# Kernel optimization log

Hardware: AMD Instinct MI355X
Metric: run time of the kernel (lower is better)

Reference implementation:

```python
import jax, jax.numpy as jnp
import numpy as np
import math

L = 16.0
DT = 1.0
TAU = 10.0
THRESHOLD = 1.0
ALPHA = 0.01
DECAY = math.exp(-DT / TAU)

@jax.custom_vjp
def multibit_spike(x):
    # forward: floor(x) clipped to [0, L]
    return jnp.clip(jnp.floor(x), 0.0, L)

def _spike_fwd(x):
    return multibit_spike(x), x

def _spike_bwd(x, g):
    dist = jnp.abs(x - jnp.round(x))
    scale = jnp.clip(1.0 - 2.0 * dist, 0.0, 1.0)
    in_range = ((x >= 0.0) & (x <= L + 1.0)).astype(g.dtype)
    return (g * in_range * scale,)

multibit_spike.defvjp(_spike_fwd, _spike_bwd)

def setup_inputs() -> dict:
    key = jax.random.key(0)
    k_x, k_w = jax.random.split(key)
    B, T, IN, H = 16, 2048, 512, 512
    # SNN-aware init: std = 0.5*threshold / (sqrt(fan_in)*0.3)
    std = 0.5 * THRESHOLD / (math.sqrt(IN) * 0.3)
    x = jax.random.normal(k_x, (B, T, IN), dtype=jnp.float32)
    W = jax.random.normal(k_w, (H, IN), dtype=jnp.float32) * std
    b = jnp.zeros((H,), dtype=jnp.float32)
    return {"x": x, "W": W, "b": b}

def reference(x, W, b):
    B, T, _ = x.shape
    Hd = W.shape[0]
    # batched linear projection of the whole sequence (compute-heavy GEMM)
    h = jnp.einsum('bti,hi->bth', x, W) + b  # [B, T, H]
    v0 = jnp.zeros((B, Hd), dtype=x.dtype)
    theta0 = jnp.full((B, Hd), THRESHOLD, dtype=x.dtype)

    def step(carry, i_t):
        v, theta = carry
        v = v * DECAY + i_t
        clamp_limit = L * theta * 2.0
        v = jnp.clip(v, -clamp_limit, clamp_limit)
        spike = multibit_spike(v / theta)
        v = v - spike * theta
        theta = theta + ALPHA * spike - ALPHA * (theta - THRESHOLD)
        return (v, theta), spike

    (v_f, theta_f), spikes_tbh = jax.lax.scan(step, (v0, theta0), jnp.swapaxes(h, 0, 1))
    spikes = jnp.swapaxes(spikes_tbh, 0, 1)  # [B, T, H]
    return spikes, v_f, theta_f
```

## Files before the change

kernel.cpp:

```cpp
#include <hip/hip_runtime.h>

#define B_  16
#define T_  2048
#define IN_ 512
#define H_  512
#define M_  (B_ * T_)

static __device__ __forceinline__ float4 ld4(const float* p) {
    return *reinterpret_cast<const float4*>(p);
}

#define BM 128
#define BN 128
#define BK 16
#define LDT (BM + 4)

__global__ __launch_bounds__(256)
void gemm_xwT(const float* __restrict__ X, const float* __restrict__ W,
              const float* __restrict__ bias, float* __restrict__ Hout) {
    __shared__ float As[BK][LDT];
    __shared__ float Bs[BK][LDT];

    const int tid = threadIdx.x;
    const int m0  = blockIdx.x * BM;
    const int n0  = blockIdx.y * BN;

    const int tx = tid & 15;
    const int ty = tid >> 4;

    const int row = tid >> 2;
    const int kph = (tid & 3) * 4;

    float acc[8][8];
#pragma unroll
    for (int i = 0; i < 8; ++i)
#pragma unroll
        for (int j = 0; j < 8; ++j) acc[i][j] = 0.0f;

    for (int k0 = 0; k0 < IN_; k0 += BK) {
        float4 a0 = ld4(&X[(size_t)(m0 + row)      * IN_ + k0 + kph]);
        float4 a1 = ld4(&X[(size_t)(m0 + row + 64) * IN_ + k0 + kph]);
        float4 b0 = ld4(&W[(size_t)(n0 + row)      * IN_ + k0 + kph]);
        float4 b1 = ld4(&W[(size_t)(n0 + row + 64) * IN_ + k0 + kph]);

        As[kph + 0][row]      = a0.x;  As[kph + 1][row]      = a0.y;
        As[kph + 2][row]      = a0.z;  As[kph + 3][row]      = a0.w;
        As[kph + 0][row + 64] = a1.x;  As[kph + 1][row + 64] = a1.y;
        As[kph + 2][row + 64] = a1.z;  As[kph + 3][row + 64] = a1.w;
        Bs[kph + 0][row]      = b0.x;  Bs[kph + 1][row]      = b0.y;
        Bs[kph + 2][row]      = b0.z;  Bs[kph + 3][row]      = b0.w;
        Bs[kph + 0][row + 64] = b1.x;  Bs[kph + 1][row + 64] = b1.y;
        Bs[kph + 2][row + 64] = b1.z;  Bs[kph + 3][row + 64] = b1.w;
        __syncthreads();

#pragma unroll
        for (int k = 0; k < BK; ++k) {
            float4 av0 = ld4(&As[k][ty * 8]);
            float4 av1 = ld4(&As[k][ty * 8 + 4]);
            float4 bv0 = ld4(&Bs[k][tx * 8]);
            float4 bv1 = ld4(&Bs[k][tx * 8 + 4]);
            const float am[8] = {av0.x, av0.y, av0.z, av0.w,
                                 av1.x, av1.y, av1.z, av1.w};
            const float bn8[8] = {bv0.x, bv0.y, bv0.z, bv0.w,
                                  bv1.x, bv1.y, bv1.z, bv1.w};
#pragma unroll
            for (int i = 0; i < 8; ++i)
#pragma unroll
                for (int j = 0; j < 8; ++j)
                    acc[i][j] = fmaf(am[i], bn8[j], acc[i][j]);
        }
        __syncthreads();
    }

    float4 bb0 = ld4(&bias[n0 + tx * 8]);
    float4 bb1 = ld4(&bias[n0 + tx * 8 + 4]);
#pragma unroll
    for (int i = 0; i < 8; ++i) {
        const int rowo = m0 + ty * 8 + i;
        float4 o0, o1;
        o0.x = acc[i][0] + bb0.x;  o0.y = acc[i][1] + bb0.y;
        o0.z = acc[i][2] + bb0.z;  o0.w = acc[i][3] + bb0.w;
        o1.x = acc[i][4] + bb1.x;  o1.y = acc[i][5] + bb1.y;
        o1.z = acc[i][6] + bb1.z;  o1.w = acc[i][7] + bb1.w;
        *reinterpret_cast<float4*>(&Hout[(size_t)rowo * H_ + n0 + tx * 8])     = o0;
        *reinterpret_cast<float4*>(&Hout[(size_t)rowo * H_ + n0 + tx * 8 + 4]) = o1;
    }
}

#define PF 16

__global__ __launch_bounds__(64)
void gif_scan(const float* __restrict__ Hbuf, float* __restrict__ spikes,
              float* __restrict__ vout, float* __restrict__ thout) {
    const int gid = blockIdx.x * 64 + threadIdx.x;
    const int b = gid >> 9;
    const int h = gid & 511;

    const float* ip = Hbuf   + (size_t)b * T_ * H_ + h;
    float*       sp = spikes + (size_t)b * T_ * H_ + h;

    const float DECAY_F = 0.9048374180359595f;
    const float ALPHA_F = 0.01f;

    float buf[PF];
#pragma unroll
    for (int j = 0; j < PF; ++j) buf[j] = ip[(size_t)j * H_];

    float v = 0.0f, theta = 1.0f;
    for (int t0 = 0; t0 < T_; t0 += PF) {
        float nbuf[PF];
        const int tnx = t0 + PF;
        if (tnx < T_) {
#pragma unroll
            for (int j = 0; j < PF; ++j) nbuf[j] = ip[(size_t)(tnx + j) * H_];
        }
#pragma unroll
        for (int j = 0; j < PF; ++j) {
            float cur = buf[j];
            v = v * DECAY_F + cur;
            float cl = 32.0f * theta;
            v = fminf(fmaxf(v, -cl), cl);
            float s = floorf(v / theta);
            s = fminf(fmaxf(s, 0.0f), 16.0f);
            v = v - s * theta;
            theta = theta + ALPHA_F * s - ALPHA_F * (theta - 1.0f);
            sp[(size_t)(t0 + j) * H_] = s;
        }
#pragma unroll
        for (int j = 0; j < PF; ++j) buf[j] = nbuf[j];
    }
    vout[gid]  = v;
    thout[gid] = theta;
}

extern "C" void kernel_launch(void* const* d_in, const int* in_sizes, int n_in,
                              void* d_out, int out_size, void* d_ws, size_t ws_size,
                              hipStream_t stream) {
    const float* x    = (const float*)d_in[0];
    const float* W    = (const float*)d_in[1];
    const float* bias = (const float*)d_in[2];

    float* out   = (float*)d_out;
    float* hbuf  = (float*)d_ws;

    float* spikes = out;
    float* v_f    = out + (size_t)B_ * T_ * H_;
    float* th_f   = v_f + (size_t)B_ * H_;

    dim3 grid(M_ / BM, H_ / BN);
    gemm_xwT<<<grid, 256, 0, stream>>>(x, W, bias, hbuf);
    gif_scan<<<(B_ * H_) / 64, 64, 0, stream>>>(hbuf, spikes, v_f, th_f);
}
```

Before: 442.4 us.

## Fuse GEMM and scan into one persistent kernel with per-chunk flag sync

Merges the GEMM and the recurrent scan into one launch. GEMM blocks are ordered by time chunk and each bumps an atomic flag when its tile is written. Scan blocks spin on those flags and process each 128-step chunk as soon as it is ready, so the serial scan overlaps the GEMM instead of waiting for it to finish. The GEMM also gains register prefetch of the next K slice and a strided thread-to-output mapping to cut LDS bank conflicts. The scheme depends on the scan blocks being co-resident, which holds only while the workspace has room for the flags; spinning scan blocks also occupy CUs that the GEMM could use.

```diff
diff --git a/kernel.cpp b/kernel.cpp
--- a/kernel.cpp
+++ b/kernel.cpp
@@ -6,24 +6,36 @@
 #define H_  512
 #define M_  (B_ * T_)
 
-static __device__ __forceinline__ float4 ld4(const float* p) {
-    return *reinterpret_cast<const float4*>(p);
-}
-
 #define BM 128
 #define BN 128
 #define BK 16
 #define LDT (BM + 4)
 
-__global__ __launch_bounds__(256)
-void gemm_xwT(const float* __restrict__ X, const float* __restrict__ W,
-              const float* __restrict__ bias, float* __restrict__ Hout) {
+#define NTAU   16
+#define TCHUNK 128
+#define GEMM_BLOCKS 1024
+#define SCAN_BLOCKS 32
+#define BLOCKS_PER_TAU 64
+
+static __device__ __forceinline__ float4 ld4(const float* p) {
+    return *reinterpret_cast<const float4*>(p);
+}
+
+__device__ __forceinline__
+void gemm_body(const float* __restrict__ X, const float* __restrict__ W,
+               const float* __restrict__ bias, float* __restrict__ Hout,
+               int gg, int* flags)
+{
     __shared__ float As[BK][LDT];
     __shared__ float Bs[BK][LDT];
 
     const int tid = threadIdx.x;
-    const int m0  = blockIdx.x * BM;
-    const int n0  = blockIdx.y * BN;
+    const int tau = gg >> 6;
+    const int idx = gg & 63;
+    const int bb  = idx >> 2;
+    const int ni  = idx & 3;
+    const int m0  = bb * 2048 + tau * TCHUNK;
+    const int n0  = ni * BN;
 
     const int tx = tid & 15;
     const int ty = tid >> 4;
@@ -31,6 +43,13 @@
     const int row = tid >> 2;
     const int kph = (tid & 3) * 4;
 
+    const float* pa0 = X + (size_t)(m0 + row) * IN_ + kph;
+    const float* pa1 = pa0 + (size_t)64 * IN_;
+    const float* pb0 = W + (size_t)(n0 + row) * IN_ + kph;
+    const float* pb1 = pb0 + (size_t)64 * IN_;
+
+    float4 ra0 = ld4(pa0), ra1 = ld4(pa1), rb0 = ld4(pb0), rb1 = ld4(pb1);
+
     float acc[8][8];
 #pragma unroll
     for (int i = 0; i < 8; ++i)
@@ -38,27 +57,27 @@
         for (int j = 0; j < 8; ++j) acc[i][j] = 0.0f;
 
     for (int k0 = 0; k0 < IN_; k0 += BK) {
-        float4 a0 = ld4(&X[(size_t)(m0 + row)      * IN_ + k0 + kph]);
-        float4 a1 = ld4(&X[(size_t)(m0 + row + 64) * IN_ + k0 + kph]);
-        float4 b0 = ld4(&W[(size_t)(n0 + row)      * IN_ + k0 + kph]);
-        float4 b1 = ld4(&W[(size_t)(n0 + row + 64) * IN_ + k0 + kph]);
-
-        As[kph + 0][row]      = a0.x;  As[kph + 1][row]      = a0.y;
-        As[kph + 2][row]      = a0.z;  As[kph + 3][row]      = a0.w;
-        As[kph + 0][row + 64] = a1.x;  As[kph + 1][row + 64] = a1.y;
-        As[kph + 2][row + 64] = a1.z;  As[kph + 3][row + 64] = a1.w;
-        Bs[kph + 0][row]      = b0.x;  Bs[kph + 1][row]      = b0.y;
-        Bs[kph + 2][row]      = b0.z;  Bs[kph + 3][row]      = b0.w;
-        Bs[kph + 0][row + 64] = b1.x;  Bs[kph + 1][row + 64] = b1.y;
-        Bs[kph + 2][row + 64] = b1.z;  Bs[kph + 3][row + 64] = b1.w;
+        As[kph + 0][row]      = ra0.x;  As[kph + 1][row]      = ra0.y;
+        As[kph + 2][row]      = ra0.z;  As[kph + 3][row]      = ra0.w;
+        As[kph + 0][row + 64] = ra1.x;  As[kph + 1][row + 64] = ra1.y;
+        As[kph + 2][row + 64] = ra1.z;  As[kph + 3][row + 64] = ra1.w;
+        Bs[kph + 0][row]      = rb0.x;  Bs[kph + 1][row]      = rb0.y;
+        Bs[kph + 2][row]      = rb0.z;  Bs[kph + 3][row]      = rb0.w;
+        Bs[kph + 0][row + 64] = rb1.x;  Bs[kph + 1][row + 64] = rb1.y;
+        Bs[kph + 2][row + 64] = rb1.z;  Bs[kph + 3][row + 64] = rb1.w;
         __syncthreads();
 
+        if (k0 + BK < IN_) {
+            ra0 = ld4(pa0 + k0 + BK);  ra1 = ld4(pa1 + k0 + BK);
+            rb0 = ld4(pb0 + k0 + BK);  rb1 = ld4(pb1 + k0 + BK);
+        }
+
 #pragma unroll
         for (int k = 0; k < BK; ++k) {
-            float4 av0 = ld4(&As[k][ty * 8]);
-            float4 av1 = ld4(&As[k][ty * 8 + 4]);
-            float4 bv0 = ld4(&Bs[k][tx * 8]);
-            float4 bv1 = ld4(&Bs[k][tx * 8 + 4]);
+            float4 av0 = ld4(&As[k][ty * 4]);
+            float4 av1 = ld4(&As[k][ty * 4 + 64]);
+            float4 bv0 = ld4(&Bs[k][tx * 4]);
+            float4 bv1 = ld4(&Bs[k][tx * 4 + 64]);
             const float am[8] = {av0.x, av0.y, av0.z, av0.w,
                                  av1.x, av1.y, av1.z, av1.w};
             const float bn8[8] = {bv0.x, bv0.y, bv0.z, bv0.w,
@@ -72,27 +91,36 @@
         __syncthreads();
     }
 
-    float4 bb0 = ld4(&bias[n0 + tx * 8]);
-    float4 bb1 = ld4(&bias[n0 + tx * 8 + 4]);
+    float4 bb0 = ld4(&bias[n0 + tx * 4]);
+    float4 bb1 = ld4(&bias[n0 + tx * 4 + 64]);
 #pragma unroll
     for (int i = 0; i < 8; ++i) {
-        const int rowo = m0 + ty * 8 + i;
+        const int r = m0 + ((i < 4) ? (ty * 4 + i) : (64 + ty * 4 + (i - 4)));
         float4 o0, o1;
         o0.x = acc[i][0] + bb0.x;  o0.y = acc[i][1] + bb0.y;
         o0.z = acc[i][2] + bb0.z;  o0.w = acc[i][3] + bb0.w;
         o1.x = acc[i][4] + bb1.x;  o1.y = acc[i][5] + bb1.y;
         o1.z = acc[i][6] + bb1.z;  o1.w = acc[i][7] + bb1.w;
-        *reinterpret_cast<float4*>(&Hout[(size_t)rowo * H_ + n0 + tx * 8])     = o0;
-        *reinterpret_cast<float4*>(&Hout[(size_t)rowo * H_ + n0 + tx * 8 + 4]) = o1;
-    }
-}
-
-#define PF 16
-
-__global__ __launch_bounds__(64)
-void gif_scan(const float* __restrict__ Hbuf, float* __restrict__ spikes,
-              float* __restrict__ vout, float* __restrict__ thout) {
-    const int gid = blockIdx.x * 64 + threadIdx.x;
+        *reinterpret_cast<float4*>(&Hout[(size_t)r * H_ + n0 + tx * 4])      = o0;
+        *reinterpret_cast<float4*>(&Hout[(size_t)r * H_ + n0 + tx * 4 + 64]) = o1;
+    }
+
+    if (flags) {
+        __threadfence();
+        __syncthreads();
+        if (tid == 0)
+            __hip_atomic_fetch_add(&flags[tau], 1, __ATOMIC_RELEASE,
+                                   __HIP_MEMORY_SCOPE_AGENT);
+    }
+}
+
+__device__ __forceinline__
+void scan_body(const float* __restrict__ Hbuf, float* __restrict__ spikes,
+               float* __restrict__ vout, float* __restrict__ thout,
+               int sb, int* flags)
+{
+    const int tid = threadIdx.x;
+    const int gid = sb * 256 + tid;
     const int b = gid >> 9;
     const int h = gid & 511;
 
@@ -102,35 +130,74 @@
     const float DECAY_F = 0.9048374180359595f;
     const float ALPHA_F = 0.01f;
 
-    float buf[PF];
-#pragma unroll
-    for (int j = 0; j < PF; ++j) buf[j] = ip[(size_t)j * H_];
-
     float v = 0.0f, theta = 1.0f;
-    for (int t0 = 0; t0 < T_; t0 += PF) {
-        float nbuf[PF];
-        const int tnx = t0 + PF;
-        if (tnx < T_) {
-#pragma unroll
-            for (int j = 0; j < PF; ++j) nbuf[j] = ip[(size_t)(tnx + j) * H_];
-        }
-#pragma unroll
-        for (int j = 0; j < PF; ++j) {
-            float cur = buf[j];
-            v = v * DECAY_F + cur;
-            float cl = 32.0f * theta;
-            v = fminf(fmaxf(v, -cl), cl);
-            float s = floorf(v / theta);
-            s = fminf(fmaxf(s, 0.0f), 16.0f);
-            v = v - s * theta;
-            theta = theta + ALPHA_F * s - ALPHA_F * (theta - 1.0f);
-            sp[(size_t)(t0 + j) * H_] = s;
-        }
-#pragma unroll
-        for (int j = 0; j < PF; ++j) buf[j] = nbuf[j];
+
+    for (int tau = 0; tau < NTAU; ++tau) {
+        if (flags) {
+            if (tid == 0) {
+                while (__hip_atomic_load(&flags[tau], __ATOMIC_ACQUIRE,
+                                         __HIP_MEMORY_SCOPE_AGENT) < BLOCKS_PER_TAU)
+                    __builtin_amdgcn_s_sleep(8);
+            }
+            __syncthreads();
+        }
+        const int tb = tau * TCHUNK;
+
+        float buf[16];
+#pragma unroll
+        for (int j = 0; j < 16; ++j) buf[j] = ip[(size_t)(tb + j) * H_];
+
+        for (int t0 = 0; t0 < TCHUNK; t0 += 16) {
+            float nbuf[16];
+            if (t0 + 16 < TCHUNK) {
+#pragma unroll
+                for (int j = 0; j < 16; ++j)
+                    nbuf[j] = ip[(size_t)(tb + t0 + 16 + j) * H_];
+            }
+#pragma unroll
+            for (int j = 0; j < 16; ++j) {
+                float cur = buf[j];
+                v = v * DECAY_F + cur;
+                float cl = 32.0f * theta;
+                v = fminf(fmaxf(v, -cl), cl);
+                float s = floorf(v / theta);
+                s = fminf(fmaxf(s, 0.0f), 16.0f);
+                v = v - s * theta;
+                theta = theta + ALPHA_F * s - ALPHA_F * (theta - 1.0f);
+                sp[(size_t)(tb + t0 + j) * H_] = s;
+            }
+#pragma unroll
+            for (int j = 0; j < 16; ++j) buf[j] = nbuf[j];
+        }
     }
     vout[gid]  = v;
     thout[gid] = theta;
+}
+
+__global__ __launch_bounds__(256)
+void fused_kernel(const float* __restrict__ X, const float* __restrict__ W,
+                  const float* __restrict__ bias, float* __restrict__ hbuf,
+                  float* __restrict__ spikes, float* __restrict__ vf,
+                  float* __restrict__ thf, int* flags)
+{
+    if ((int)blockIdx.x < SCAN_BLOCKS)
+        scan_body(hbuf, spikes, vf, thf, blockIdx.x, flags);
+    else
+        gemm_body(X, W, bias, hbuf, blockIdx.x - SCAN_BLOCKS, flags);
+}
+
+__global__ __launch_bounds__(256)
+void gemm_kernel(const float* __restrict__ X, const float* __restrict__ W,
+                 const float* __restrict__ bias, float* __restrict__ hbuf)
+{
+    gemm_body(X, W, bias, hbuf, blockIdx.x, nullptr);
+}
+
+__global__ __launch_bounds__(256)
+void scan_kernel(const float* __restrict__ hbuf, float* __restrict__ spikes,
+                 float* __restrict__ vf, float* __restrict__ thf)
+{
+    scan_body(hbuf, spikes, vf, thf, blockIdx.x, nullptr);
 }
 
 extern "C" void kernel_launch(void* const* d_in, const int* in_sizes, int n_in,
@@ -140,14 +207,21 @@
     const float* W    = (const float*)d_in[1];
     const float* bias = (const float*)d_in[2];
 
-    float* out   = (float*)d_out;
-    float* hbuf  = (float*)d_ws;
-
+    float* out    = (float*)d_out;
     float* spikes = out;
-    float* v_f    = out + (size_t)B_ * T_ * H_;
+    float* v_f    = out + (size_t)M_ * H_;
     float* th_f   = v_f + (size_t)B_ * H_;
 
-    dim3 grid(M_ / BM, H_ / BN);
-    gemm_xwT<<<grid, 256, 0, stream>>>(x, W, bias, hbuf);
-    gif_scan<<<(B_ * H_) / 64, 64, 0, stream>>>(hbuf, spikes, v_f, th_f);
-}
+    float* hbuf   = (float*)d_ws;
+    const size_t hbytes = (size_t)M_ * H_ * sizeof(float);
+
+    if (ws_size >= hbytes + 256) {
+        int* flags = (int*)((char*)d_ws + hbytes);
+        hipMemsetAsync(flags, 0, NTAU * sizeof(int), stream);
+        fused_kernel<<<SCAN_BLOCKS + GEMM_BLOCKS, 256, 0, stream>>>(
+            x, W, bias, hbuf, spikes, v_f, th_f, flags);
+    } else {
+        gemm_kernel<<<GEMM_BLOCKS, 256, 0, stream>>>(x, W, bias, hbuf);
+        scan_kernel<<<SCAN_BLOCKS, 256, 0, stream>>>(hbuf, spikes, v_f, th_f);
+    }
+}
```

Measured after the change: 483.0 us. 1.09x slower.
